# Performance work log

Hardware: AMD Instinct MI355X
Metric: run time of the kernel (lower is better)

The kernel has to match this reference:

```python
import jax, jax.numpy as jnp
import numpy as np

D_MODEL = 1024
N_HEAD = 16
D_HEAD = D_MODEL // N_HEAD
D_FF = 4096
B, S = 2, 2048
EPS = 1e-5


def setup_inputs() -> dict:
    key = jax.random.key(0)
    ks = jax.random.split(key, 16)
    sc = 1.0 / np.sqrt(D_MODEL)
    x = jax.random.normal(ks[0], (B, S, D_MODEL), dtype=jnp.float32)
    # causal mask: 1 where attention is disallowed (upper triangle)
    mask = jnp.triu(jnp.ones((S, S), dtype=jnp.int32), k=1)[None, None]
    p = {
        'x': x,
        'mask': mask,
        'wq': jax.random.normal(ks[1], (D_MODEL, D_MODEL), jnp.float32) * sc,
        'bq': jnp.zeros((D_MODEL,), jnp.float32),
        'wk': jax.random.normal(ks[2], (D_MODEL, D_MODEL), jnp.float32) * sc,
        'bk': jnp.zeros((D_MODEL,), jnp.float32),
        'wv': jax.random.normal(ks[3], (D_MODEL, D_MODEL), jnp.float32) * sc,
        'bv': jnp.zeros((D_MODEL,), jnp.float32),
        'wo': jax.random.normal(ks[4], (D_MODEL, D_MODEL), jnp.float32) * sc,
        'bo': jnp.zeros((D_MODEL,), jnp.float32),
        'w1': jax.random.normal(ks[5], (D_MODEL, D_FF), jnp.float32) * sc,
        'b1': jnp.zeros((D_FF,), jnp.float32),
        'w2': jax.random.normal(ks[6], (D_FF, D_MODEL), jnp.float32) * (1.0 / np.sqrt(D_FF)),
        'b2': jnp.zeros((D_MODEL,), jnp.float32),
        'g1': jnp.ones((D_MODEL,), jnp.float32),
        'beta1': jnp.zeros((D_MODEL,), jnp.float32),
        'g2': jnp.ones((D_MODEL,), jnp.float32),
        'beta2': jnp.zeros((D_MODEL,), jnp.float32),
    }
    return p


def _layer_norm(x, g, b):
    mu = jnp.mean(x, axis=-1, keepdims=True)
    var = jnp.mean(jnp.square(x - mu), axis=-1, keepdims=True)
    return (x - mu) * jax.lax.rsqrt(var + EPS) * g + b


def reference(x, mask, wq, bq, wk, bk, wv, bv, wo, bo, w1, b1, w2, b2, g1, beta1, g2, beta2):
    b, s, _ = x.shape
    # QKV projections -> [B, H, S, Dh]
    q = (x @ wq + bq).reshape(b, s, N_HEAD, D_HEAD).transpose(0, 2, 1, 3)
    k = (x @ wk + bk).reshape(b, s, N_HEAD, D_HEAD).transpose(0, 2, 1, 3)
    v = (x @ wv + bv).reshape(b, s, N_HEAD, D_HEAD).transpose(0, 2, 1, 3)
    scores = jnp.einsum('bhqd,bhkd->bhqk', q, k) / np.sqrt(D_HEAD)  # [B,H,S,S]
    scores = jnp.where(mask == 1, -jnp.inf, scores)
    attn = jax.nn.softmax(scores, axis=-1)
    out = jnp.einsum('bhqk,bhkd->bhqd', attn, v)
    out = out.transpose(0, 2, 1, 3).reshape(b, s, D_MODEL)
    attn_out = out @ wo + bo
    x1 = _layer_norm(x + attn_out, g1, beta1)
    ffn = jax.nn.relu(x1 @ w1 + b1) @ w2 + b2
    return _layer_norm(x1 + ffn, g2, beta2)
```

## Files before the change

### kernel.cpp

```cpp
#include <hip/hip_runtime.h>
#include <hip/hip_bf16.h>
#include <cstdint>

#define D_MODEL 1024
#define D_FF    4096
#define NHEAD   16
#define DHEAD   64
#define BATCH   2
#define SEQ     2048
#define BT      (BATCH*SEQ)
#define QKVLD   (3*D_MODEL)
#define LN_EPS  1e-5f

typedef __bf16 bf16_t;
typedef bf16_t bf16x8 __attribute__((ext_vector_type(8)));
typedef float  f32x4  __attribute__((ext_vector_type(4)));

__device__ __forceinline__ unsigned short f2b(float f){
  bf16_t h = (bf16_t)f;
  return __builtin_bit_cast(unsigned short, h);
}

__device__ __forceinline__ void gload16(const void* g, void* l){
  __builtin_amdgcn_global_load_lds(
      (const __attribute__((address_space(1))) unsigned int*)g,
      (__attribute__((address_space(3))) unsigned int*)l, 16, 0, 0);
}

__global__ __launch_bounds__(256) void cvt_f32_bf16(
    const float* __restrict__ in, unsigned short* __restrict__ out, int n){
  int i = (blockIdx.x*256 + threadIdx.x)*4;
  if (i < n){
    float4 v = *(const float4*)(in + i);
    ushort4 u; u.x=f2b(v.x); u.y=f2b(v.y); u.z=f2b(v.z); u.w=f2b(v.w);
    *(ushort4*)(out + i) = u;
  }
}

__global__ __launch_bounds__(256) void concat_bias(
    const float* __restrict__ bq, const float* __restrict__ bk,
    const float* __restrict__ bv, float* __restrict__ o){
  int i = blockIdx.x*256 + threadIdx.x;
  if (i < D_MODEL){ o[i]=bq[i]; o[D_MODEL+i]=bk[i]; o[2*D_MODEL+i]=bv[i]; }
}

__global__ __launch_bounds__(256) void transpose_cvt(
    const float* __restrict__ in, unsigned short* __restrict__ out, int R, int C){
  __shared__ float t[32][33];
  int c0 = blockIdx.x*32, r0 = blockIdx.y*32;
  int tx = threadIdx.x, ty = threadIdx.y;
  #pragma unroll
  for (int i=0;i<4;++i){ int r = ty + i*8; t[r][tx] = in[(size_t)(r0+r)*C + c0+tx]; }
  __syncthreads();
  #pragma unroll
  for (int i=0;i<4;++i){ int r = ty + i*8; out[(size_t)(c0+r)*R + r0+tx] = f2b(t[tx][r]); }
}

__global__ __launch_bounds__(256) void transpose_v(
    const unsigned short* __restrict__ QKV, unsigned short* __restrict__ Vt){
  __shared__ unsigned short t[32][33];
  int s0 = blockIdx.x*32, d0 = blockIdx.y*32, bh = blockIdx.z;
  int b = bh>>4, h = bh&15;
  int tx = threadIdx.x, ty = threadIdx.y;
  #pragma unroll
  for (int i=0;i<4;++i){ int r = ty + i*8;
    t[r][tx] = QKV[(size_t)(b*SEQ + s0+r)*QKVLD + 2*D_MODEL + h*DHEAD + d0+tx]; }
  __syncthreads();
  #pragma unroll
  for (int i=0;i<4;++i){ int r = ty + i*8;
    Vt[((size_t)bh*DHEAD + d0+r)*SEQ + s0+tx] = t[tx][r]; }
}

template<int EPI>
__global__ __launch_bounds__(512,4) void gemm128(
    const unsigned short* __restrict__ A, const unsigned short* __restrict__ Bt,
    const float* __restrict__ bias, const float* __restrict__ resid,
    float* __restrict__ outF, unsigned short* __restrict__ outB,
    int M, int N, int K){
  __shared__ __attribute__((aligned(16))) unsigned short As[2][128*64];
  __shared__ __attribute__((aligned(16))) unsigned short Bs[2][128*64];
  int tid = threadIdx.x;
  int lane = tid & 63, wave = tid >> 6;
  int lr = lane & 15, lg = lane >> 4;
  int row0 = blockIdx.x*128, col0 = blockIdx.y*128;
  int wr = (wave>>2)*64, wc = (wave&3)*32;
  int x7 = lr & 7;

  int sr = tid >> 3;
  int sl = (tid & 7) ^ (sr & 7);
  auto STAGE = [&](int k0, int buf){
    #pragma unroll
    for (int it=0; it<2; ++it){
      int c = it*512 + tid;
      int r = it*64 + sr;
      gload16(A  + (size_t)(row0+r)*K + k0 + sl*8, &As[buf][c<<3]);
      gload16(Bt + (size_t)(col0+r)*K + k0 + sl*8, &Bs[buf][c<<3]);
    }
  };

  f32x4 acc[4][2] = {};
  int nk = K >> 6;
  STAGE(0, 0);
  asm volatile("s_waitcnt vmcnt(0)" ::: "memory");
  __builtin_amdgcn_s_barrier();
  int cur = 0;
  for (int t=0; t<nk; ++t){
    if (t+1 < nk) STAGE((t+1)<<6, cur^1);
    #pragma unroll
    for (int kk=0; kk<2; ++kk){
      int sk = ((kk*4 + lg) ^ x7) << 3;
      bf16x8 af[4], bfr[2];
      #pragma unroll
      for (int mi=0;mi<4;++mi) af[mi]  = *(const bf16x8*)&As[cur][(wr+mi*16+lr)*64 + sk];
      #pragma unroll
      for (int ni=0;ni<2;++ni) bfr[ni] = *(const bf16x8*)&Bs[cur][(wc+ni*16+lr)*64 + sk];
      #pragma unroll
      for (int mi=0;mi<4;++mi)
        #pragma unroll
        for (int ni=0;ni<2;++ni)
          acc[mi][ni] = __builtin_amdgcn_mfma_f32_16x16x32_bf16(af[mi], bfr[ni], acc[mi][ni], 0,0,0);
    }
    asm volatile("s_waitcnt vmcnt(0)" ::: "memory");
    __builtin_amdgcn_s_barrier();
    cur ^= 1;
  }
  #pragma unroll
  for (int mi=0;mi<4;++mi){
    int row = row0 + wr + mi*16 + (lg<<2);
    #pragma unroll
    for (int ni=0;ni<2;++ni){
      int col = col0 + wc + ni*16 + lr;
      float bs = bias[col];
      #pragma unroll
      for (int j=0;j<4;++j){
        size_t idx = (size_t)(row+j)*N + col;
        float v = acc[mi][ni][j] + bs;
        if (EPI==1){ v += resid[idx]; outF[idx] = v; }
        else if (EPI==2){ v = fmaxf(v, 0.f); outB[idx] = f2b(v); }
        else { outB[idx] = f2b(v); }
      }
    }
  }
}

__global__ __launch_bounds__(256,2) void attn_k(
    const unsigned short* __restrict__ QKV,
    const unsigned short* __restrict__ Vt, unsigned short* __restrict__ O){
  __shared__ __attribute__((aligned(16))) unsigned short Ks[2][128*64];
  __shared__ __attribute__((aligned(16))) unsigned short Vs[2][64*128];
  __shared__ __attribute__((aligned(16))) unsigned short Ps[4][16*128];
  int tid = threadIdx.x, lane = tid&63, wave = tid>>6;
  int lr = lane&15, lg = lane>>4;
  int bid = blockIdx.x;
  int L = (bid & 7)*64 + (bid >> 3);
  int qx = L & 15;
  int bh = L >> 4;
  int b = bh>>4, h = bh&15;
  const int NT = SEQ/64;

  #pragma unroll 1
  for (int half=0; half<2; ++half){
    int qt = half ? qx : (NT-1 - qx);
    int q0w = qt*64 + wave*16;

    const unsigned short* Qrow = QKV + (size_t)(b*SEQ + q0w + lr)*QKVLD + h*DHEAD;
    bf16x8 qf[2];
    qf[0] = *(const bf16x8*)(Qrow + lg*8);
    qf[1] = *(const bf16x8*)(Qrow + 32 + lg*8);

    f32x4 oacc[4] = {};
    float m_run[4], l_run[4];
    #pragma unroll
    for (int j=0;j<4;++j){ m_run[j] = -1e30f; l_run[j] = 0.f; }

    auto STAGE = [&](int t, int buf){
      int kv0 = t*128;
      #pragma unroll
      for (int it=0; it<4; ++it){
        int c = it*256 + tid;
        int rk = c>>3, slk = (c&7) ^ (rk&7);
        gload16(QKV + (size_t)(b*SEQ + kv0 + rk)*QKVLD + D_MODEL + h*DHEAD + slk*8, &Ks[buf][c<<3]);
        int rv = c>>4, slv = (c&15) ^ (rv&15);
        gload16(Vt + ((size_t)bh*DHEAD + rv)*SEQ + kv0 + slv*8, &Vs[buf][c<<3]);
      }
    };

    int nkv = (qt + 2) >> 1;
    STAGE(0, 0);
    asm volatile("s_waitcnt vmcnt(0)" ::: "memory");
    __builtin_amdgcn_s_barrier();
    int cur = 0;
    for (int t=0; t<nkv; ++t){
      if (t+1 < nkv) STAGE(t+1, cur^1);

      int kv0 = t*128;
      f32x4 sacc[8] = {};
      #pragma unroll
      for (int kk=0;kk<2;++kk){
        #pragma unroll
        for (int ni=0;ni<8;++ni){
          int krow = ni*16 + lr;
          bf16x8 kf = *(const bf16x8*)&Ks[cur][krow*64 + (((kk*4+lg) ^ (krow&7))<<3)];
          sacc[ni] = __builtin_amdgcn_mfma_f32_16x16x32_bf16(qf[kk], kf, sacc[ni], 0,0,0);
        }
      }
      if (t == nkv-1){
        #pragma unroll
        for (int ni=0;ni<8;++ni){
          f32x4 v = sacc[ni];
          int kpos = kv0 + ni*16 + lr;
          #pragma unroll
          for (int j=0;j<4;++j){
            int qpos = q0w + lg*4 + j;
            float sv = v[j]*0.125f;
            v[j] = (kpos > qpos) ? -1e30f : sv;
          }
          sacc[ni] = v;
        }
      } else {
        #pragma unroll
        for (int ni=0;ni<8;++ni) sacc[ni] *= 0.125f;
      }
      #pragma unroll
      for (int j=0;j<4;++j){
        float rm = -1e30f;
        #pragma unroll
        for (int ni=0;ni<8;++ni) rm = fmaxf(rm, sacc[ni][j]);
        #pragma unroll
        for (int d=1; d<16; d<<=1) rm = fmaxf(rm, __shfl_xor(rm, d, 16));
        float mnew = fmaxf(m_run[j], rm);
        float corr = __expf(m_run[j] - mnew);
        m_run[j] = mnew;
        float rs_ = 0.f;
        #pragma unroll
        for (int ni=0;ni<8;++ni){
          float p = __expf(sacc[ni][j] - mnew);
          sacc[ni][j] = p;
          rs_ += p;
        }
        #pragma unroll
        for (int d=1; d<16; d<<=1) rs_ += __shfl_xor(rs_, d, 16);
        l_run[j] = l_run[j]*corr + rs_;
        #pragma unroll
        for (int nd=0; nd<4; ++nd) oacc[nd][j] *= corr;
      }
      #pragma unroll
      for (int ni=0;ni<8;++ni)
        #pragma unroll
        for (int j=0;j<4;++j){
          int qrow = lg*4 + j;
          int kcol = ni*16 + lr;
          int slot = (kcol>>3) ^ (qrow&15);
          Ps[wave][qrow*128 + slot*8 + (kcol&7)] = f2b(sacc[ni][j]);
        }
      #pragma unroll
      for (int kk=0;kk<4;++kk){
        bf16x8 pa = *(const bf16x8*)&Ps[wave][lr*128 + (((kk*4+lg) ^ (lr&15))<<3)];
        #pragma unroll
        for (int nd=0; nd<4; ++nd){
          int dr = nd*16 + lr;
          bf16x8 vf = *(const bf16x8*)&Vs[cur][dr*128 + (((kk*4+lg) ^ (dr&15))<<3)];
          oacc[nd] = __builtin_amdgcn_mfma_f32_16x16x32_bf16(pa, vf, oacc[nd], 0,0,0);
        }
      }
      asm volatile("s_waitcnt vmcnt(0)" ::: "memory");
      __builtin_amdgcn_s_barrier();
      cur ^= 1;
    }
    #pragma unroll
    for (int j=0;j<4;++j){
      float inv = 1.f / l_run[j];
      int token = b*SEQ + q0w + lg*4 + j;
      #pragma unroll
      for (int nd=0; nd<4; ++nd)
        O[(size_t)token*D_MODEL + h*DHEAD + nd*16 + lr] = f2b(oacc[nd][j]*inv);
    }
  }
}

template<int MODE>
__global__ __launch_bounds__(256) void ln_k(
    const float* __restrict__ in, const float* __restrict__ g, const float* __restrict__ bta,
    float* __restrict__ outF, unsigned short* __restrict__ outB){
  int row = blockIdx.x, tid = threadIdx.x;
  float4 v = ((const float4*)(in + (size_t)row*D_MODEL))[tid];
  float s = v.x+v.y+v.z+v.w;
  float q = v.x*v.x+v.y*v.y+v.z*v.z+v.w*v.w;
  #pragma unroll
  for (int d=32; d; d>>=1){ s += __shfl_xor(s, d); q += __shfl_xor(q, d); }
  __shared__ float rs[4], rq[4];
  int wave = tid>>6;
  if ((tid&63)==0){ rs[wave]=s; rq[wave]=q; }
  __syncthreads();
  s = rs[0]+rs[1]+rs[2]+rs[3];
  q = rq[0]+rq[1]+rq[2]+rq[3];
  float mu  = s * (1.f/D_MODEL);
  float var = q * (1.f/D_MODEL) - mu*mu;
  float rstd = rsqrtf(var + LN_EPS);
  float4 gg = ((const float4*)g)[tid];
  float4 bb = ((const float4*)bta)[tid];
  float o0 = (v.x-mu)*rstd*gg.x + bb.x;
  float o1 = (v.y-mu)*rstd*gg.y + bb.y;
  float o2 = (v.z-mu)*rstd*gg.z + bb.z;
  float o3 = (v.w-mu)*rstd*gg.w + bb.w;
  float4 o; o.x=o0; o.y=o1; o.z=o2; o.w=o3;
  ((float4*)(outF + (size_t)row*D_MODEL))[tid] = o;
  if (MODE==0){
    ushort4 u; u.x=f2b(o0); u.y=f2b(o1); u.z=f2b(o2); u.w=f2b(o3);
    ((ushort4*)(outB + (size_t)row*D_MODEL))[tid] = u;
  }
}

extern "C" void kernel_launch(void* const* d_in, const int* in_sizes, int n_in,
                              void* d_out, int out_size, void* d_ws, size_t ws_size,
                              hipStream_t stream){
  const float* x  = (const float*)d_in[0];
  const float* wq = (const float*)d_in[2];  const float* bq = (const float*)d_in[3];
  const float* wk = (const float*)d_in[4];  const float* bk = (const float*)d_in[5];
  const float* wv = (const float*)d_in[6];  const float* bv = (const float*)d_in[7];
  const float* wo = (const float*)d_in[8];  const float* bo = (const float*)d_in[9];
  const float* w1 = (const float*)d_in[10]; const float* b1 = (const float*)d_in[11];
  const float* w2 = (const float*)d_in[12]; const float* b2 = (const float*)d_in[13];
  const float* g1 = (const float*)d_in[14]; const float* be1= (const float*)d_in[15];
  const float* g2 = (const float*)d_in[16]; const float* be2= (const float*)d_in[17];

  char* w = (char*)d_ws;
  size_t off = 0;
  auto nxt = [&](size_t bytes)->void*{
    void* p = w + off; off = (off + bytes + 255) & ~(size_t)255; return p;
  };
  unsigned short* xb    = (unsigned short*)nxt((size_t)BT*D_MODEL*2);
  unsigned short* wqkvT = (unsigned short*)nxt((size_t)QKVLD*D_MODEL*2);
  unsigned short* woT   = (unsigned short*)nxt((size_t)D_MODEL*D_MODEL*2);
  unsigned short* w1T   = (unsigned short*)nxt((size_t)D_MODEL*D_FF*2);
  unsigned short* w2T   = (unsigned short*)nxt((size_t)D_MODEL*D_FF*2);
  float*          bqkv  = (float*)nxt((size_t)QKVLD*4);
  unsigned short* QKV   = (unsigned short*)nxt((size_t)BT*QKVLD*2);
  unsigned short* VtG   = (unsigned short*)nxt((size_t)BT*D_MODEL*2);
  unsigned short* attnb = (unsigned short*)nxt((size_t)BT*D_MODEL*2);
  float*          hbuf  = (float*)nxt((size_t)BT*D_MODEL*4);
  float*          x1f   = (float*)nxt((size_t)BT*D_MODEL*4);
  unsigned short* ffn1  = (unsigned short*)nxt((size_t)BT*D_FF*2);
  unsigned short* x1b   = attnb;
  float*          h2    = hbuf;

  dim3 tb(32,8);
  cvt_f32_bf16<<<(BT*D_MODEL)/1024, 256, 0, stream>>>(x, xb, BT*D_MODEL);
  concat_bias<<<4, 256, 0, stream>>>(bq, bk, bv, bqkv);
  transpose_cvt<<<dim3(D_MODEL/32, D_MODEL/32), tb, 0, stream>>>(wq, wqkvT,                    D_MODEL, D_MODEL);
  transpose_cvt<<<dim3(D_MODEL/32, D_MODEL/32), tb, 0, stream>>>(wk, wqkvT + D_MODEL*D_MODEL,  D_MODEL, D_MODEL);
  transpose_cvt<<<dim3(D_MODEL/32, D_MODEL/32), tb, 0, stream>>>(wv, wqkvT + 2*D_MODEL*D_MODEL,D_MODEL, D_MODEL);
  transpose_cvt<<<dim3(D_MODEL/32, D_MODEL/32), tb, 0, stream>>>(wo, woT, D_MODEL, D_MODEL);
  transpose_cvt<<<dim3(D_FF/32,    D_MODEL/32), tb, 0, stream>>>(w1, w1T, D_MODEL, D_FF);
  transpose_cvt<<<dim3(D_MODEL/32, D_FF/32),    tb, 0, stream>>>(w2, w2T, D_FF, D_MODEL);

  gemm128<0><<<dim3(BT/128, QKVLD/128), 512, 0, stream>>>(xb, wqkvT, bqkv, nullptr, nullptr, QKV, BT, QKVLD, D_MODEL);

  transpose_v<<<dim3(SEQ/32, DHEAD/32, BATCH*NHEAD), tb, 0, stream>>>(QKV, VtG);
  attn_k<<<512, 256, 0, stream>>>(QKV, VtG, attnb);

  gemm128<1><<<dim3(BT/128, D_MODEL/128), 512, 0, stream>>>(attnb, woT, bo, x, hbuf, nullptr, BT, D_MODEL, D_MODEL);
  ln_k<0><<<BT, 256, 0, stream>>>(hbuf, g1, be1, x1f, x1b);
  gemm128<2><<<dim3(BT/128, D_FF/128), 512, 0, stream>>>(x1b, w1T, b1, nullptr, nullptr, ffn1, BT, D_FF, D_MODEL);
  gemm128<1><<<dim3(BT/128, D_MODEL/128), 512, 0, stream>>>(ffn1, w2T, b2, x1f, h2, nullptr, BT, D_MODEL, D_FF);
  ln_k<1><<<BT, 256, 0, stream>>>(h2, g2, be2, (float*)d_out, nullptr);
}
```

Before: 256.5 us.

## Split-K the N=1024 GEMMs and fuse partial sum, bias, residual into LayerNorm

The two GEMMs with N=1024 (output projection and FFN down-projection) now run as split-K with two K halves along blockIdx.z. Each half writes an fp32 partial into a scratch buffer that reuses the QKV allocation. The LayerNorm kernel now sums both partials, adds bias and residual, then normalizes. This doubles the grid from 256 to 512 blocks to fill more CUs, at the cost of extra fp32 partial traffic (two full M×N writes and reads).

```diff
diff --git a/kernel.cpp b/kernel.cpp
--- a/kernel.cpp
+++ b/kernel.cpp
@@ -100,12 +100,14 @@
 
   f32x4 acc[4][2] = {};
   int nk = K >> 6;
-  STAGE(0, 0);
+  int t0 = 0, t1 = nk;
+  if (EPI==3){ int half = nk >> 1; t0 = blockIdx.z*half; t1 = t0 + half; }
+  STAGE(t0<<6, 0);
   asm volatile("s_waitcnt vmcnt(0)" ::: "memory");
   __builtin_amdgcn_s_barrier();
   int cur = 0;
-  for (int t=0; t<nk; ++t){
-    if (t+1 < nk) STAGE((t+1)<<6, cur^1);
+  for (int t=t0; t<t1; ++t){
+    if (t+1 < t1) STAGE((t+1)<<6, cur^1);
     #pragma unroll
     for (int kk=0; kk<2; ++kk){
       int sk = ((kk*4 + lg) ^ x7) << 3;
@@ -124,18 +126,19 @@
     __builtin_amdgcn_s_barrier();
     cur ^= 1;
   }
+  float* outP = (EPI==3) ? (outF + (size_t)blockIdx.z*((size_t)M*N)) : outF;
   #pragma unroll
   for (int mi=0;mi<4;++mi){
     int row = row0 + wr + mi*16 + (lg<<2);
     #pragma unroll
     for (int ni=0;ni<2;++ni){
       int col = col0 + wc + ni*16 + lr;
-      float bs = bias[col];
+      float bs = (EPI==3) ? 0.f : bias[col];
       #pragma unroll
       for (int j=0;j<4;++j){
         size_t idx = (size_t)(row+j)*N + col;
         float v = acc[mi][ni][j] + bs;
-        if (EPI==1){ v += resid[idx]; outF[idx] = v; }
+        if (EPI==3){ outP[idx] = v; }
         else if (EPI==2){ v = fmaxf(v, 0.f); outB[idx] = f2b(v); }
         else { outB[idx] = f2b(v); }
       }
@@ -279,11 +282,21 @@
 }
 
 template<int MODE>
-__global__ __launch_bounds__(256) void ln_k(
-    const float* __restrict__ in, const float* __restrict__ g, const float* __restrict__ bta,
+__global__ __launch_bounds__(256) void ln_sum_k(
+    const float* __restrict__ P,
+    const float* __restrict__ bias,
+    const float* __restrict__ resid,
+    const float* __restrict__ g, const float* __restrict__ bta,
     float* __restrict__ outF, unsigned short* __restrict__ outB){
   int row = blockIdx.x, tid = threadIdx.x;
-  float4 v = ((const float4*)(in + (size_t)row*D_MODEL))[tid];
+  const size_t MN = (size_t)BT*D_MODEL;
+  float4 p0 = ((const float4*)(P + (size_t)row*D_MODEL))[tid];
+  float4 p1 = ((const float4*)(P + MN + (size_t)row*D_MODEL))[tid];
+  float4 rr = ((const float4*)(resid + (size_t)row*D_MODEL))[tid];
+  float4 bb = ((const float4*)bias)[tid];
+  float4 v;
+  v.x = p0.x+p1.x+bb.x+rr.x; v.y = p0.y+p1.y+bb.y+rr.y;
+  v.z = p0.z+p1.z+bb.z+rr.z; v.w = p0.w+p1.w+bb.w+rr.w;
   float s = v.x+v.y+v.z+v.w;
   float q = v.x*v.x+v.y*v.y+v.z*v.z+v.w*v.w;
   #pragma unroll
@@ -298,11 +311,11 @@
   float var = q * (1.f/D_MODEL) - mu*mu;
   float rstd = rsqrtf(var + LN_EPS);
   float4 gg = ((const float4*)g)[tid];
-  float4 bb = ((const float4*)bta)[tid];
-  float o0 = (v.x-mu)*rstd*gg.x + bb.x;
-  float o1 = (v.y-mu)*rstd*gg.y + bb.y;
-  float o2 = (v.z-mu)*rstd*gg.z + bb.z;
-  float o3 = (v.w-mu)*rstd*gg.w + bb.w;
+  float4 be = ((const float4*)bta)[tid];
+  float o0 = (v.x-mu)*rstd*gg.x + be.x;
+  float o1 = (v.y-mu)*rstd*gg.y + be.y;
+  float o2 = (v.z-mu)*rstd*gg.z + be.z;
+  float o3 = (v.w-mu)*rstd*gg.w + be.w;
   float4 o; o.x=o0; o.y=o1; o.z=o2; o.w=o3;
   ((float4*)(outF + (size_t)row*D_MODEL))[tid] = o;
   if (MODE==0){
@@ -338,11 +351,10 @@
   unsigned short* QKV   = (unsigned short*)nxt((size_t)BT*QKVLD*2);
   unsigned short* VtG   = (unsigned short*)nxt((size_t)BT*D_MODEL*2);
   unsigned short* attnb = (unsigned short*)nxt((size_t)BT*D_MODEL*2);
-  float*          hbuf  = (float*)nxt((size_t)BT*D_MODEL*4);
   float*          x1f   = (float*)nxt((size_t)BT*D_MODEL*4);
   unsigned short* ffn1  = (unsigned short*)nxt((size_t)BT*D_FF*2);
+  float*          Psum  = (float*)QKV;
   unsigned short* x1b   = attnb;
-  float*          h2    = hbuf;
 
   dim3 tb(32,8);
   cvt_f32_bf16<<<(BT*D_MODEL)/1024, 256, 0, stream>>>(x, xb, BT*D_MODEL);
@@ -359,9 +371,11 @@
   transpose_v<<<dim3(SEQ/32, DHEAD/32, BATCH*NHEAD), tb, 0, stream>>>(QKV, VtG);
   attn_k<<<512, 256, 0, stream>>>(QKV, VtG, attnb);
 
-  gemm128<1><<<dim3(BT/128, D_MODEL/128), 512, 0, stream>>>(attnb, woT, bo, x, hbuf, nullptr, BT, D_MODEL, D_MODEL);
-  ln_k<0><<<BT, 256, 0, stream>>>(hbuf, g1, be1, x1f, x1b);
+  gemm128<3><<<dim3(BT/128, D_MODEL/128, 2), 512, 0, stream>>>(attnb, woT, nullptr, nullptr, Psum, nullptr, BT, D_MODEL, D_MODEL);
+  ln_sum_k<0><<<BT, 256, 0, stream>>>(Psum, bo, x, g1, be1, x1f, x1b);
+
   gemm128<2><<<dim3(BT/128, D_FF/128), 512, 0, stream>>>(x1b, w1T, b1, nullptr, nullptr, ffn1, BT, D_FF, D_MODEL);
-  gemm128<1><<<dim3(BT/128, D_MODEL/128), 512, 0, stream>>>(ffn1, w2T, b2, x1f, h2, nullptr, BT, D_MODEL, D_FF);
-  ln_k<1><<<BT, 256, 0, stream>>>(h2, g2, be2, (float*)d_out, nullptr);
-}
+
+  gemm128<3><<<dim3(BT/128, D_MODEL/128, 2), 512, 0, stream>>>(ffn1, w2T, nullptr, nullptr, Psum, nullptr, BT, D_MODEL, D_FF);
+  ln_sum_k<1><<<BT, 256, 0, stream>>>(Psum, b2, x1f, g2, be2, (float*)d_out, nullptr);
+}
```

Result: faster. 238.2 us (-7.1%).
